# Kernel optimization log

Measured on AMD Instinct MI355X. Metric: run time of the kernel, lower is better.

Reference implementation:

```python
import jax, jax.numpy as jnp
import numpy as np

HEADS = 4
EPS = 1e-5

def _layernorm(x, g, b):
    mu = jnp.mean(x, axis=-1, keepdims=True)
    var = jnp.var(x, axis=-1, keepdims=True)
    return (x - mu) / jnp.sqrt(var + EPS) * g + b

def setup_inputs() -> dict:
    key = jax.random.key(0)
    ks = jax.random.split(key, 16)
    N, dim, k, G = 400000, 256, 1, 4096
    h = jax.random.normal(ks[0], (N, dim), dtype=jnp.float32)
    batch = jnp.sort(jax.random.randint(ks[1], (N,), 0, G).astype(jnp.int64))
    s = 1.0 / np.sqrt(dim)
    return {
        "h": h,
        "batch": batch,
        "num_graphs": G,
        "seed": jax.random.normal(ks[2], (k, dim), dtype=jnp.float32),
        "in_proj_w": jax.random.uniform(ks[3], (3 * dim, dim), minval=-s, maxval=s, dtype=jnp.float32),
        "in_proj_b": jnp.zeros((3 * dim,), jnp.float32),
        "out_w": jax.random.uniform(ks[4], (dim, dim), minval=-s, maxval=s, dtype=jnp.float32),
        "out_b": jnp.zeros((dim,), jnp.float32),
        "w1": jax.random.uniform(ks[5], (4 * dim, dim), minval=-s, maxval=s, dtype=jnp.float32),
        "b1": jnp.zeros((4 * dim,), jnp.float32),
        "w2": jax.random.uniform(ks[6], (dim, 4 * dim), minval=-1.0 / np.sqrt(4 * dim), maxval=1.0 / np.sqrt(4 * dim), dtype=jnp.float32),
        "b2": jnp.zeros((dim,), jnp.float32),
        "g1": jnp.ones((dim,), jnp.float32),
        "beta1": jnp.zeros((dim,), jnp.float32),
        "g2": jnp.ones((dim,), jnp.float32),
        "beta2": jnp.zeros((dim,), jnp.float32),
    }

def reference(h, batch, num_graphs, seed, in_proj_w, in_proj_b, out_w, out_b,
              w1, b1, w2, b2, g1, beta1, g2, beta2):
    N, dim = h.shape
    k = seed.shape[0]
    hd = dim // HEADS
    G = num_graphs
    # q/k/v projections (torch MHA packed in_proj: rows [0:dim]=Q, [dim:2dim]=K, [2dim:]=V)
    q = seed @ in_proj_w[:dim].T + in_proj_b[:dim]                 # [k, dim]
    kk = h @ in_proj_w[dim:2 * dim].T + in_proj_b[dim:2 * dim]     # [N, dim]
    vv = h @ in_proj_w[2 * dim:].T + in_proj_b[2 * dim:]           # [N, dim]
    qh = q.reshape(k, HEADS, hd).transpose(1, 0, 2)                # [H, k, hd]
    kh = kk.reshape(N, HEADS, hd)                                  # [N, H, hd]
    vh = vv.reshape(N, HEADS, hd)                                  # [N, H, hd]
    scale = 1.0 / np.sqrt(hd)
    scores = jnp.einsum('hkd,nhd->nhk', qh, kh) * scale            # [N, H, k]
    # segment softmax over nodes of each graph
    smax = jax.ops.segment_max(scores, batch, num_segments=G)      # [G, H, k]
    e = jnp.exp(scores - smax[batch])                              # [N, H, k]
    denom = jax.ops.segment_sum(e, batch, num_segments=G)          # [G, H, k]
    wv = jax.ops.segment_sum(e[:, :, :, None] * vh[:, :, None, :], batch, num_segments=G)  # [G, H, k, hd]
    attn = jnp.where(denom[..., None] > 0, wv / jnp.maximum(denom, 1e-9)[..., None], 0.0)
    attn = attn.transpose(0, 2, 1, 3).reshape(G, k, dim)           # [G, k, dim]
    o = attn @ out_w.T + out_b                                     # [G, k, dim]
    x = _layernorm(o + seed[None, :, :], g1, beta1)
    f = jax.nn.relu(x @ w1.T + b1) @ w2.T + b2
    x = _layernorm(x + f, g2, beta2)
    # empty graphs output zeros (matches torch loop)
    count = jax.ops.segment_sum(jnp.ones((N,), jnp.float32), batch, num_segments=G)
    return jnp.where((count > 0)[:, None, None], x, 0.0)
```

## Files before the change

### kernel.cpp

```cpp
#include <hip/hip_runtime.h>
#include <hip/hip_bf16.h>


#define DIM 256
#define CHUNK 16

typedef short bf16x8 __attribute__((ext_vector_type(8)));
typedef float f32x4  __attribute__((ext_vector_type(4)));
#define MFMA16(a, b, c) __builtin_amdgcn_mfma_f32_16x16x32_bf16(a, b, c, 0, 0, 0)

#define GLOAD_LDS16(gp, lp)                                          \
    __builtin_amdgcn_global_load_lds(                                \
        (const __attribute__((address_space(1))) void*)(gp),         \
        (__attribute__((address_space(3))) void*)(lp), 16, 0, 0)

#define OFF_C      0
#define OFF_D      1024
#define OFF_CONST  1040
#define OFF_P2B    2048
#define OFF_W1B    133120
#define OFF_W2B    264192
#define OFF_TB     395264
#define OFF_CNT    6162432
#define OFF_STARTS 6166528

__global__ __launch_bounds__(256) void prep_all_kernel(
    const float* __restrict__ seed, const float* __restrict__ ipw,
    const float* __restrict__ ipb, const float* __restrict__ out_w,
    const float* __restrict__ out_b, const float* __restrict__ w1,
    const float* __restrict__ w2, const int* __restrict__ batch,
    float* __restrict__ cvec, float* __restrict__ dconst,
    float* __restrict__ constvec, __hip_bfloat16* __restrict__ P2b,
    __hip_bfloat16* __restrict__ w1b, __hip_bfloat16* __restrict__ w2b,
    int* __restrict__ starts, int N, int G)
{
    int b = blockIdx.x, t = threadIdx.x;
    __shared__ float q_s[DIM];
    if (b < 1024) {
        int i = b >> 2, hD = b & 3;
        float a = 0.f;
        for (int j = 0; j < 64; ++j)
            a += out_w[i * DIM + hD * 64 + j]
               * ipw[(size_t)(2 * DIM + hD * 64 + j) * DIM + t];
        P2b[(size_t)i * 1024 + hD * DIM + t] = __float2bfloat16(a);
    } else if (b == 1024) {
        const float scale = 0.125f;
        float acc = ipb[t];
        for (int d = 0; d < DIM; ++d) acc += seed[d] * ipw[t * DIM + d];
        q_s[t] = acc;
        __syncthreads();
        for (int hh = 0; hh < 4; ++hh) {
            float a = 0.f;
            for (int j = 0; j < 64; ++j)
                a += q_s[hh * 64 + j] * ipw[(size_t)(DIM + hh * 64 + j) * DIM + t];
            cvec[hh * DIM + t] = a * scale;
        }
        if (t < 4) {
            float a = 0.f;
            for (int j = 0; j < 64; ++j)
                a += q_s[t * 64 + j] * ipb[DIM + t * 64 + j];
            dconst[t] = a * scale;
        }
        float cc = out_b[t];
        for (int c = 0; c < DIM; ++c)
            cc += out_w[t * DIM + c] * ipb[2 * DIM + c];
        constvec[t] = cc;
    } else if (b < 1153) {
        int base = (b - 1025) * 2048 + t;
        for (int i = 0; i < 8; ++i)
            w1b[base + i * 256] = __float2bfloat16(w1[base + i * 256]);
    } else if (b < 1281) {
        int base = (b - 1153) * 2048 + t;
        for (int i = 0; i < 8; ++i)
            w2b[base + i * 256] = __float2bfloat16(w2[base + i * 256]);
    } else {
        int n = (b - 1281) * 256 + t;
        if (n < N) {
            int bn = batch[n];
            int bp = (n == 0) ? -1 : batch[n - 1];
            for (int gg = bp + 1; gg <= bn; ++gg) starts[gg] = n;
            if (n == N - 1)
                for (int gg = bn + 1; gg <= G; ++gg) starts[gg] = N;
        }
    }
}

__global__ __launch_bounds__(256) void attn_pool_kernel(
    const float* __restrict__ hmat, const int* __restrict__ starts,
    const float* __restrict__ cvec, const float* __restrict__ dconst,
    __hip_bfloat16* __restrict__ Tb, int* __restrict__ cnt)
{
    int g = blockIdx.x;
    int tid = threadIdx.x;
    int lane = tid & 63, wave = tid >> 6;

    __shared__ float hbuf[4][2][4][DIM];
    __shared__ float lred[4][4];

    int s = starts[g], e = starts[g + 1];
    if (tid == 0) cnt[g] = e - s;
    size_t tbase = (size_t)g * 1024;
    if (e == s) {
        __hip_bfloat16 z = __float2bfloat16(0.f);
        Tb[tbase + tid] = z; Tb[tbase + 256 + tid] = z;
        Tb[tbase + 512 + tid] = z; Tb[tbase + 768 + tid] = z;
        return;
    }

    int hh = lane & 3, seg = lane >> 2;
    const float* cb = cvec + hh * DIM + seg * 16;
    float4 cr0 = *(const float4*)(cb + 0);
    float4 cr1 = *(const float4*)(cb + 4);
    float4 cr2 = *(const float4*)(cb + 8);
    float4 cr3 = *(const float4*)(cb + 12);
    float dc_mine = dconst[hh];

    float S00 = 0.f, S01 = 0.f, S02 = 0.f, S03 = 0.f;
    float S10 = 0.f, S11 = 0.f, S12 = 0.f, S13 = 0.f;
    float S20 = 0.f, S21 = 0.f, S22 = 0.f, S23 = 0.f;
    float S30 = 0.f, S31 = 0.f, S32 = 0.f, S33 = 0.f;
    float lp = 0.f;

    int rows0 = wave * 4;

#pragma unroll
    for (int i = 0; i < 4; ++i) {
        int r = min(s + rows0 + i, e - 1);
        GLOAD_LDS16(&hmat[(size_t)r * DIM + lane * 4], &hbuf[wave][0][i][0]);
    }

    int cur = 0;
    for (int n0 = s; n0 < e; n0 += CHUNK, cur ^= 1) {
        int ccnt = min(CHUNK, e - n0);
        int n1 = n0 + CHUNK;
#pragma unroll
        for (int i = 0; i < 4; ++i) {
            int r = min(n1 + rows0 + i, e - 1);
            GLOAD_LDS16(&hmat[(size_t)r * DIM + lane * 4],
                        &hbuf[wave][cur ^ 1][i][0]);
        }
        asm volatile("s_waitcnt vmcnt(4)" ::: "memory");
        __builtin_amdgcn_sched_barrier(0);

        int nmine = min(max(ccnt - rows0, 0), 4);
        for (int j = 0; j < nmine; ++j) {
            const float* hb = &hbuf[wave][cur][j][0];
            const float* hs = hb + seg * 16;
            float4 h0 = *(const float4*)(hs + 0);
            float4 h1 = *(const float4*)(hs + 4);
            float4 h2 = *(const float4*)(hs + 8);
            float4 h3 = *(const float4*)(hs + 12);
            float p = h0.x * cr0.x + h0.y * cr0.y + h0.z * cr0.z + h0.w * cr0.w
                    + h1.x * cr1.x + h1.y * cr1.y + h1.z * cr1.z + h1.w * cr1.w
                    + h2.x * cr2.x + h2.y * cr2.y + h2.z * cr2.z + h2.w * cr2.w
                    + h3.x * cr3.x + h3.y * cr3.y + h3.z * cr3.z + h3.w * cr3.w;
            p += __shfl_xor(p, 4);
            p += __shfl_xor(p, 8);
            p += __shfl_xor(p, 16);
            p += __shfl_xor(p, 32);
            float ev = __expf(p + dc_mine);
            lp += ev;
            float e0 = __shfl(ev, 0), e1 = __shfl(ev, 1);
            float e2 = __shfl(ev, 2), e3 = __shfl(ev, 3);
            float v0 = hb[lane], v1 = hb[64 + lane];
            float v2 = hb[128 + lane], v3 = hb[192 + lane];
            S00 = fmaf(e0, v0, S00); S01 = fmaf(e0, v1, S01);
            S02 = fmaf(e0, v2, S02); S03 = fmaf(e0, v3, S03);
            S10 = fmaf(e1, v0, S10); S11 = fmaf(e1, v1, S11);
            S12 = fmaf(e1, v2, S12); S13 = fmaf(e1, v3, S13);
            S20 = fmaf(e2, v0, S20); S21 = fmaf(e2, v1, S21);
            S22 = fmaf(e2, v2, S22); S23 = fmaf(e2, v3, S23);
            S30 = fmaf(e3, v0, S30); S31 = fmaf(e3, v1, S31);
            S32 = fmaf(e3, v2, S32); S33 = fmaf(e3, v3, S33);
        }
    }

    asm volatile("s_waitcnt vmcnt(0)" ::: "memory");
    __builtin_amdgcn_sched_barrier(0);
    __syncthreads();
    float* part = &hbuf[0][0][0][0];
#define PIDX(w_, h_, c_) ((((w_) * 4 + (h_)) * 4 + (c_)) * 64 + lane)
    part[PIDX(wave, 0, 0)] = S00; part[PIDX(wave, 0, 1)] = S01;
    part[PIDX(wave, 0, 2)] = S02; part[PIDX(wave, 0, 3)] = S03;
    part[PIDX(wave, 1, 0)] = S10; part[PIDX(wave, 1, 1)] = S11;
    part[PIDX(wave, 1, 2)] = S12; part[PIDX(wave, 1, 3)] = S13;
    part[PIDX(wave, 2, 0)] = S20; part[PIDX(wave, 2, 1)] = S21;
    part[PIDX(wave, 2, 2)] = S22; part[PIDX(wave, 2, 3)] = S23;
    part[PIDX(wave, 3, 0)] = S30; part[PIDX(wave, 3, 1)] = S31;
    part[PIDX(wave, 3, 2)] = S32; part[PIDX(wave, 3, 3)] = S33;
#undef PIDX
    if (lane < 4) lred[wave][lane] = lp;
    __syncthreads();

    int cg = tid >> 6, ln = tid & 63;
#pragma unroll
    for (int h = 0; h < 4; ++h) {
        int base = (h * 4 + cg) * 64 + ln;
        float sum = part[base] + part[base + 1024]
                  + part[base + 2048] + part[base + 3072];
        float den = lred[0][h] + lred[1][h] + lred[2][h] + lred[3][h];
        Tb[tbase + h * 256 + tid] = __float2bfloat16(sum / den);
    }
}

__global__ __launch_bounds__(1024) void mlp_fused_kernel(
    const __hip_bfloat16* __restrict__ Tb, const __hip_bfloat16* __restrict__ P2b,
    const float* __restrict__ constvec, const float* __restrict__ seed,
    const float* __restrict__ g1, const float* __restrict__ be1,
    const __hip_bfloat16* __restrict__ w1b, const float* __restrict__ b1,
    const __hip_bfloat16* __restrict__ w2b, const float* __restrict__ b2,
    const float* __restrict__ g2, const float* __restrict__ be2,
    const int* __restrict__ cnt, float* __restrict__ outp)
{
    int m0 = blockIdx.x * 16;
    int tid = threadIdx.x;
    int w = tid >> 6, lane = tid & 63, quad = lane >> 4, l16 = lane & 15;

    __shared__ float x1s[16][260];
    __shared__ __hip_bfloat16 x1bs[16][264];
    __shared__ __hip_bfloat16 us[16][1032];
    __shared__ float redS[16][16], redQ[16][16];

    f32x4 acc0 = (f32x4){0.f, 0.f, 0.f, 0.f};
    const __hip_bfloat16* Ap0 = Tb + (size_t)(m0 + l16) * 1024 + quad * 8;
    const __hip_bfloat16* Bp0 = P2b + (size_t)(w * 16 + l16) * 1024 + quad * 8;
#pragma unroll 4
    for (int k0 = 0; k0 < 1024; k0 += 32) {
        bf16x8 a = *(const bf16x8*)(Ap0 + k0);
        bf16x8 b = *(const bf16x8*)(Bp0 + k0);
        acc0 = MFMA16(a, b, acc0);
    }
    float v0[4];
    {
        int col = w * 16 + l16;
        float cv = constvec[col] + seed[col];
        float sum[4], sq[4];
#pragma unroll
        for (int r = 0; r < 4; ++r) {
            float x = acc0[r] + cv;
            v0[r] = x; sum[r] = x; sq[r] = x * x;
        }
#pragma unroll
        for (int r = 0; r < 4; ++r) {
            float s_ = sum[r], q_ = sq[r];
            s_ += __shfl_xor(s_, 1);  q_ += __shfl_xor(q_, 1);
            s_ += __shfl_xor(s_, 2);  q_ += __shfl_xor(q_, 2);
            s_ += __shfl_xor(s_, 4);  q_ += __shfl_xor(q_, 4);
            s_ += __shfl_xor(s_, 8);  q_ += __shfl_xor(q_, 8);
            if (l16 == 0) { redS[w][quad * 4 + r] = s_; redQ[w][quad * 4 + r] = q_; }
        }
    }
    __syncthreads();
    {
        float mu_r[4], rs_r[4];
#pragma unroll
        for (int r = 0; r < 4; ++r) {
            int row = quad * 4 + r;
            float s_ = 0.f, q_ = 0.f;
#pragma unroll
            for (int ww = 0; ww < 16; ++ww) { s_ += redS[ww][row]; q_ += redQ[ww][row]; }
            float mu = s_ * (1.f / 256);
            float var = q_ * (1.f / 256) - mu * mu;
            mu_r[r] = mu;
            rs_r[r] = rsqrtf(fmaxf(var, 0.f) + 1e-5f);
        }
        int col = w * 16 + l16;
        float gg = g1[col], bb = be1[col];
#pragma unroll
        for (int r = 0; r < 4; ++r) {
            int row = quad * 4 + r;
            float y = (v0[r] - mu_r[r]) * rs_r[r] * gg + bb;
            x1s[row][col] = y;
            x1bs[row][col] = __float2bfloat16(y);
        }
    }
    __syncthreads();

    f32x4 acc1[4];
#pragma unroll
    for (int i = 0; i < 4; ++i) acc1[i] = (f32x4){0.f, 0.f, 0.f, 0.f};
    const __hip_bfloat16* Bp1 = w1b + (size_t)(w * 64 + l16) * 256 + quad * 8;
#pragma unroll
    for (int k0 = 0; k0 < 256; k0 += 32) {
        bf16x8 a = *(const bf16x8*)&x1bs[l16][quad * 8 + k0];
#pragma unroll
        for (int nt = 0; nt < 4; ++nt) {
            bf16x8 b = *(const bf16x8*)(Bp1 + (size_t)nt * 16 * 256 + k0);
            acc1[nt] = MFMA16(a, b, acc1[nt]);
        }
    }
#pragma unroll
    for (int nt = 0; nt < 4; ++nt) {
        int col = w * 64 + nt * 16 + l16;
        float bb = b1[col];
#pragma unroll
        for (int r = 0; r < 4; ++r) {
            int row = quad * 4 + r;
            us[row][col] = __float2bfloat16(fmaxf(acc1[nt][r] + bb, 0.f));
        }
    }
    __syncthreads();

    f32x4 acc2 = (f32x4){0.f, 0.f, 0.f, 0.f};
    const __hip_bfloat16* Bp2 = w2b + (size_t)(w * 16 + l16) * 1024 + quad * 8;
#pragma unroll 4
    for (int k0 = 0; k0 < 1024; k0 += 32) {
        bf16x8 a = *(const bf16x8*)&us[l16][quad * 8 + k0];
        bf16x8 b = *(const bf16x8*)(Bp2 + k0);
        acc2 = MFMA16(a, b, acc2);
    }
    float v2[4];
    {
        int col = w * 16 + l16;
        float bb = b2[col];
        float sum[4], sq[4];
#pragma unroll
        for (int r = 0; r < 4; ++r) {
            int row = quad * 4 + r;
            float x = acc2[r] + bb + x1s[row][col];
            v2[r] = x; sum[r] = x; sq[r] = x * x;
        }
#pragma unroll
        for (int r = 0; r < 4; ++r) {
            float s_ = sum[r], q_ = sq[r];
            s_ += __shfl_xor(s_, 1);  q_ += __shfl_xor(q_, 1);
            s_ += __shfl_xor(s_, 2);  q_ += __shfl_xor(q_, 2);
            s_ += __shfl_xor(s_, 4);  q_ += __shfl_xor(q_, 4);
            s_ += __shfl_xor(s_, 8);  q_ += __shfl_xor(q_, 8);
            if (l16 == 0) { redS[w][quad * 4 + r] = s_; redQ[w][quad * 4 + r] = q_; }
        }
    }
    __syncthreads();
    {
        int col = w * 16 + l16;
        float gg = g2[col], bb = be2[col];
#pragma unroll
        for (int r = 0; r < 4; ++r) {
            int row = quad * 4 + r;
            float s_ = 0.f, q_ = 0.f;
#pragma unroll
            for (int ww = 0; ww < 16; ++ww) { s_ += redS[ww][row]; q_ += redQ[ww][row]; }
            float mu = s_ * (1.f / 256);
            float var = q_ * (1.f / 256) - mu * mu;
            float rs = rsqrtf(fmaxf(var, 0.f) + 1e-5f);
            int gr = m0 + row;
            float mask = (cnt[gr] > 0) ? 1.f : 0.f;
            float y = ((v2[r] - mu) * rs * gg + bb) * mask;
            outp[(size_t)gr * 256 + col] = y;
        }
    }
}

extern "C" void kernel_launch(void* const* d_in, const int* in_sizes, int n_in,
                              void* d_out, int out_size, void* d_ws, size_t ws_size,
                              hipStream_t stream) {
    const float* h     = (const float*)d_in[0];
    const int*   batch = (const int*)d_in[1];
    const float* seed  = (const float*)d_in[3];
    const float* ipw   = (const float*)d_in[4];
    const float* ipb   = (const float*)d_in[5];
    const float* out_w = (const float*)d_in[6];
    const float* out_b = (const float*)d_in[7];
    const float* w1    = (const float*)d_in[8];
    const float* b1    = (const float*)d_in[9];
    const float* w2    = (const float*)d_in[10];
    const float* b2    = (const float*)d_in[11];
    const float* g1    = (const float*)d_in[12];
    const float* be1   = (const float*)d_in[13];
    const float* g2    = (const float*)d_in[14];
    const float* be2   = (const float*)d_in[15];

    int N = in_sizes[1];
    int G = out_size / DIM;

    float* ws = (float*)d_ws;
    float* cvec     = ws + OFF_C;
    float* dconst   = ws + OFF_D;
    float* constvec = ws + OFF_CONST;
    __hip_bfloat16* P2b = (__hip_bfloat16*)(ws + OFF_P2B);
    __hip_bfloat16* w1b = (__hip_bfloat16*)(ws + OFF_W1B);
    __hip_bfloat16* w2b = (__hip_bfloat16*)(ws + OFF_W2B);
    __hip_bfloat16* Tb  = (__hip_bfloat16*)(ws + OFF_TB);
    int*   cnt      = (int*)(ws + OFF_CNT);
    int*   startsp  = (int*)(ws + OFF_STARTS);

    int sblocks = (N + 255) / 256;
    prep_all_kernel<<<1281 + sblocks, 256, 0, stream>>>(
        seed, ipw, ipb, out_w, out_b, w1, w2, batch,
        cvec, dconst, constvec, P2b, w1b, w2b, startsp, N, G);
    attn_pool_kernel<<<G, 256, 0, stream>>>(h, startsp, cvec, dconst, Tb, cnt);
    mlp_fused_kernel<<<G / 16, 1024, 0, stream>>>(Tb, P2b, constvec, seed, g1, be1,
                                                  w1b, b1, w2b, b2, g2, be2, cnt,
                                                  (float*)d_out);
}
```

Before: 666.0 us.

## Replace per-graph attention pooling with row-parallel scatter using atomics

The per-graph pooling kernel (one block per graph, LDS double-buffered loads, starts computed from batch) is replaced by a row-parallel kernel. Each wave streams 64 consecutive rows, computes all four head scores per row and accumulates exp-weighted sums in registers. It flushes them with atomicAdd to global per-graph accumulators whenever the graph id changes. A small finalize kernel divides by the denominators and writes the bf16 T matrix, and the prep kernel now zeroes the accumulators instead of building segment starts. The aim is to remove load imbalance across uneven graph sizes and the per-graph block overhead. In exchange it adds atomic traffic, leaves only one row load in flight per wave, and makes the summation order non-deterministic.

```diff
diff --git a/kernel.cpp b/kernel.cpp
--- a/kernel.cpp
+++ b/kernel.cpp
@@ -3,16 +3,10 @@
 
 
 #define DIM 256
-#define CHUNK 16
 
 typedef short bf16x8 __attribute__((ext_vector_type(8)));
 typedef float f32x4  __attribute__((ext_vector_type(4)));
 #define MFMA16(a, b, c) __builtin_amdgcn_mfma_f32_16x16x32_bf16(a, b, c, 0, 0, 0)
-
-#define GLOAD_LDS16(gp, lp)                                          \
-    __builtin_amdgcn_global_load_lds(                                \
-        (const __attribute__((address_space(1))) void*)(gp),         \
-        (__attribute__((address_space(3))) void*)(lp), 16, 0, 0)
 
 #define OFF_C      0
 #define OFF_D      1024
@@ -22,17 +16,18 @@
 #define OFF_W2B    264192
 #define OFF_TB     395264
 #define OFF_CNT    6162432
-#define OFF_STARTS 6166528
+#define OFF_SACC   6171648
+#define OFF_DEN    10365952
 
 __global__ __launch_bounds__(256) void prep_all_kernel(
     const float* __restrict__ seed, const float* __restrict__ ipw,
     const float* __restrict__ ipb, const float* __restrict__ out_w,
     const float* __restrict__ out_b, const float* __restrict__ w1,
-    const float* __restrict__ w2, const int* __restrict__ batch,
+    const float* __restrict__ w2,
     float* __restrict__ cvec, float* __restrict__ dconst,
     float* __restrict__ constvec, __hip_bfloat16* __restrict__ P2b,
     __hip_bfloat16* __restrict__ w1b, __hip_bfloat16* __restrict__ w2b,
-    int* __restrict__ starts, int N, int G)
+    float* __restrict__ zbase)
 {
     int b = blockIdx.x, t = threadIdx.x;
     __shared__ float q_s[DIM];
@@ -74,133 +69,110 @@
         for (int i = 0; i < 8; ++i)
             w2b[base + i * 256] = __float2bfloat16(w2[base + i * 256]);
     } else {
-        int n = (b - 1281) * 256 + t;
-        if (n < N) {
-            int bn = batch[n];
-            int bp = (n == 0) ? -1 : batch[n - 1];
-            for (int gg = bp + 1; gg <= bn; ++gg) starts[gg] = n;
-            if (n == N - 1)
-                for (int gg = bn + 1; gg <= G; ++gg) starts[gg] = N;
-        }
-    }
-}
-
-__global__ __launch_bounds__(256) void attn_pool_kernel(
-    const float* __restrict__ hmat, const int* __restrict__ starts,
+        int zb = b - 1281;
+        float4* z = (float4*)zbase + (size_t)zb * 1024;
+        float4 zero = {0.f, 0.f, 0.f, 0.f};
+        z[t] = zero; z[t + 256] = zero; z[t + 512] = zero; z[t + 768] = zero;
+    }
+}
+
+__global__ __launch_bounds__(256) void attn_scatter_kernel(
+    const float* __restrict__ hmat, const int* __restrict__ batch,
     const float* __restrict__ cvec, const float* __restrict__ dconst,
+    float* __restrict__ Sacc, float* __restrict__ denomAcc, int N)
+{
+    int wglob = blockIdx.x * 4 + (threadIdx.x >> 6);
+    int lane = threadIdx.x & 63;
+    int r0 = wglob * 64;
+    if (r0 >= N) return;
+    int rend = min(r0 + 64, N);
+
+    float4 c0 = *(const float4*)&cvec[0 * DIM + 4 * lane];
+    float4 c1 = *(const float4*)&cvec[1 * DIM + 4 * lane];
+    float4 c2 = *(const float4*)&cvec[2 * DIM + 4 * lane];
+    float4 c3 = *(const float4*)&cvec[3 * DIM + 4 * lane];
+    float d0 = dconst[0], d1 = dconst[1], d2 = dconst[2], d3 = dconst[3];
+
+    float4 S0 = {0,0,0,0}, S1 = {0,0,0,0}, S2 = {0,0,0,0}, S3 = {0,0,0,0};
+    float4 lp = {0,0,0,0};
+
+    int gcur = batch[r0];
+    float4 h4 = *(const float4*)&hmat[(size_t)r0 * DIM + 4 * lane];
+
+    for (int r = r0; r < rend; ++r) {
+        float4 hv = h4;
+        int gn = -1;
+        if (r + 1 < rend) {
+            gn = batch[r + 1];
+            h4 = *(const float4*)&hmat[(size_t)(r + 1) * DIM + 4 * lane];
+        }
+        float p0 = hv.x*c0.x + hv.y*c0.y + hv.z*c0.z + hv.w*c0.w;
+        float p1 = hv.x*c1.x + hv.y*c1.y + hv.z*c1.z + hv.w*c1.w;
+        float p2 = hv.x*c2.x + hv.y*c2.y + hv.z*c2.z + hv.w*c2.w;
+        float p3 = hv.x*c3.x + hv.y*c3.y + hv.z*c3.z + hv.w*c3.w;
+        float sA = __shfl_xor((lane & 1) ? p0 : p2, 1);
+        float sB = __shfl_xor((lane & 1) ? p1 : p3, 1);
+        float a  = (lane & 1) ? (p2 + sA) : (p0 + sA);
+        float bb = (lane & 1) ? (p3 + sB) : (p1 + sB);
+        float sC = __shfl_xor((lane & 2) ? a : bb, 2);
+        float v  = (lane & 2) ? (bb + sC) : (a + sC);
+        v += __shfl_xor(v, 4);
+        v += __shfl_xor(v, 8);
+        v += __shfl_xor(v, 16);
+        v += __shfl_xor(v, 32);
+        int q0 = lane & ~3;
+        float sc0 = __shfl(v, q0 + 0);
+        float sc2 = __shfl(v, q0 + 1);
+        float sc1 = __shfl(v, q0 + 2);
+        float sc3 = __shfl(v, q0 + 3);
+        float e0 = __expf(sc0 + d0), e1 = __expf(sc1 + d1);
+        float e2 = __expf(sc2 + d2), e3 = __expf(sc3 + d3);
+        lp.x += e0; lp.y += e1; lp.z += e2; lp.w += e3;
+        S0.x = fmaf(e0, hv.x, S0.x); S0.y = fmaf(e0, hv.y, S0.y);
+        S0.z = fmaf(e0, hv.z, S0.z); S0.w = fmaf(e0, hv.w, S0.w);
+        S1.x = fmaf(e1, hv.x, S1.x); S1.y = fmaf(e1, hv.y, S1.y);
+        S1.z = fmaf(e1, hv.z, S1.z); S1.w = fmaf(e1, hv.w, S1.w);
+        S2.x = fmaf(e2, hv.x, S2.x); S2.y = fmaf(e2, hv.y, S2.y);
+        S2.z = fmaf(e2, hv.z, S2.z); S2.w = fmaf(e2, hv.w, S2.w);
+        S3.x = fmaf(e3, hv.x, S3.x); S3.y = fmaf(e3, hv.y, S3.y);
+        S3.z = fmaf(e3, hv.z, S3.z); S3.w = fmaf(e3, hv.w, S3.w);
+
+        if (gn != gcur) {
+            float* base = Sacc + (size_t)gcur * 1024 + 4 * lane;
+            atomicAdd(base + 0,       S0.x); atomicAdd(base + 1,       S0.y);
+            atomicAdd(base + 2,       S0.z); atomicAdd(base + 3,       S0.w);
+            atomicAdd(base + 256 + 0, S1.x); atomicAdd(base + 256 + 1, S1.y);
+            atomicAdd(base + 256 + 2, S1.z); atomicAdd(base + 256 + 3, S1.w);
+            atomicAdd(base + 512 + 0, S2.x); atomicAdd(base + 512 + 1, S2.y);
+            atomicAdd(base + 512 + 2, S2.z); atomicAdd(base + 512 + 3, S2.w);
+            atomicAdd(base + 768 + 0, S3.x); atomicAdd(base + 768 + 1, S3.y);
+            atomicAdd(base + 768 + 2, S3.z); atomicAdd(base + 768 + 3, S3.w);
+            if (lane < 4) {
+                float lv = (lane == 0) ? lp.x : (lane == 1) ? lp.y
+                         : (lane == 2) ? lp.z : lp.w;
+                atomicAdd(denomAcc + gcur * 4 + lane, lv);
+            }
+            S0 = (float4){0,0,0,0}; S1 = (float4){0,0,0,0};
+            S2 = (float4){0,0,0,0}; S3 = (float4){0,0,0,0};
+            lp = (float4){0,0,0,0};
+            gcur = gn;
+        }
+    }
+}
+
+__global__ __launch_bounds__(256) void finalize_T_kernel(
+    const float* __restrict__ Sacc, const float* __restrict__ denomAcc,
     __hip_bfloat16* __restrict__ Tb, int* __restrict__ cnt)
 {
-    int g = blockIdx.x;
-    int tid = threadIdx.x;
-    int lane = tid & 63, wave = tid >> 6;
-
-    __shared__ float hbuf[4][2][4][DIM];
-    __shared__ float lred[4][4];
-
-    int s = starts[g], e = starts[g + 1];
-    if (tid == 0) cnt[g] = e - s;
-    size_t tbase = (size_t)g * 1024;
-    if (e == s) {
-        __hip_bfloat16 z = __float2bfloat16(0.f);
-        Tb[tbase + tid] = z; Tb[tbase + 256 + tid] = z;
-        Tb[tbase + 512 + tid] = z; Tb[tbase + 768 + tid] = z;
-        return;
-    }
-
-    int hh = lane & 3, seg = lane >> 2;
-    const float* cb = cvec + hh * DIM + seg * 16;
-    float4 cr0 = *(const float4*)(cb + 0);
-    float4 cr1 = *(const float4*)(cb + 4);
-    float4 cr2 = *(const float4*)(cb + 8);
-    float4 cr3 = *(const float4*)(cb + 12);
-    float dc_mine = dconst[hh];
-
-    float S00 = 0.f, S01 = 0.f, S02 = 0.f, S03 = 0.f;
-    float S10 = 0.f, S11 = 0.f, S12 = 0.f, S13 = 0.f;
-    float S20 = 0.f, S21 = 0.f, S22 = 0.f, S23 = 0.f;
-    float S30 = 0.f, S31 = 0.f, S32 = 0.f, S33 = 0.f;
-    float lp = 0.f;
-
-    int rows0 = wave * 4;
-
-#pragma unroll
-    for (int i = 0; i < 4; ++i) {
-        int r = min(s + rows0 + i, e - 1);
-        GLOAD_LDS16(&hmat[(size_t)r * DIM + lane * 4], &hbuf[wave][0][i][0]);
-    }
-
-    int cur = 0;
-    for (int n0 = s; n0 < e; n0 += CHUNK, cur ^= 1) {
-        int ccnt = min(CHUNK, e - n0);
-        int n1 = n0 + CHUNK;
-#pragma unroll
-        for (int i = 0; i < 4; ++i) {
-            int r = min(n1 + rows0 + i, e - 1);
-            GLOAD_LDS16(&hmat[(size_t)r * DIM + lane * 4],
-                        &hbuf[wave][cur ^ 1][i][0]);
-        }
-        asm volatile("s_waitcnt vmcnt(4)" ::: "memory");
-        __builtin_amdgcn_sched_barrier(0);
-
-        int nmine = min(max(ccnt - rows0, 0), 4);
-        for (int j = 0; j < nmine; ++j) {
-            const float* hb = &hbuf[wave][cur][j][0];
-            const float* hs = hb + seg * 16;
-            float4 h0 = *(const float4*)(hs + 0);
-            float4 h1 = *(const float4*)(hs + 4);
-            float4 h2 = *(const float4*)(hs + 8);
-            float4 h3 = *(const float4*)(hs + 12);
-            float p = h0.x * cr0.x + h0.y * cr0.y + h0.z * cr0.z + h0.w * cr0.w
-                    + h1.x * cr1.x + h1.y * cr1.y + h1.z * cr1.z + h1.w * cr1.w
-                    + h2.x * cr2.x + h2.y * cr2.y + h2.z * cr2.z + h2.w * cr2.w
-                    + h3.x * cr3.x + h3.y * cr3.y + h3.z * cr3.z + h3.w * cr3.w;
-            p += __shfl_xor(p, 4);
-            p += __shfl_xor(p, 8);
-            p += __shfl_xor(p, 16);
-            p += __shfl_xor(p, 32);
-            float ev = __expf(p + dc_mine);
-            lp += ev;
-            float e0 = __shfl(ev, 0), e1 = __shfl(ev, 1);
-            float e2 = __shfl(ev, 2), e3 = __shfl(ev, 3);
-            float v0 = hb[lane], v1 = hb[64 + lane];
-            float v2 = hb[128 + lane], v3 = hb[192 + lane];
-            S00 = fmaf(e0, v0, S00); S01 = fmaf(e0, v1, S01);
-            S02 = fmaf(e0, v2, S02); S03 = fmaf(e0, v3, S03);
-            S10 = fmaf(e1, v0, S10); S11 = fmaf(e1, v1, S11);
-            S12 = fmaf(e1, v2, S12); S13 = fmaf(e1, v3, S13);
-            S20 = fmaf(e2, v0, S20); S21 = fmaf(e2, v1, S21);
-            S22 = fmaf(e2, v2, S22); S23 = fmaf(e2, v3, S23);
-            S30 = fmaf(e3, v0, S30); S31 = fmaf(e3, v1, S31);
-            S32 = fmaf(e3, v2, S32); S33 = fmaf(e3, v3, S33);
-        }
-    }
-
-    asm volatile("s_waitcnt vmcnt(0)" ::: "memory");
-    __builtin_amdgcn_sched_barrier(0);
-    __syncthreads();
-    float* part = &hbuf[0][0][0][0];
-#define PIDX(w_, h_, c_) ((((w_) * 4 + (h_)) * 4 + (c_)) * 64 + lane)
-    part[PIDX(wave, 0, 0)] = S00; part[PIDX(wave, 0, 1)] = S01;
-    part[PIDX(wave, 0, 2)] = S02; part[PIDX(wave, 0, 3)] = S03;
-    part[PIDX(wave, 1, 0)] = S10; part[PIDX(wave, 1, 1)] = S11;
-    part[PIDX(wave, 1, 2)] = S12; part[PIDX(wave, 1, 3)] = S13;
-    part[PIDX(wave, 2, 0)] = S20; part[PIDX(wave, 2, 1)] = S21;
-    part[PIDX(wave, 2, 2)] = S22; part[PIDX(wave, 2, 3)] = S23;
-    part[PIDX(wave, 3, 0)] = S30; part[PIDX(wave, 3, 1)] = S31;
-    part[PIDX(wave, 3, 2)] = S32; part[PIDX(wave, 3, 3)] = S33;
-#undef PIDX
-    if (lane < 4) lred[wave][lane] = lp;
-    __syncthreads();
-
-    int cg = tid >> 6, ln = tid & 63;
-#pragma unroll
-    for (int h = 0; h < 4; ++h) {
-        int base = (h * 4 + cg) * 64 + ln;
-        float sum = part[base] + part[base + 1024]
-                  + part[base + 2048] + part[base + 3072];
-        float den = lred[0][h] + lred[1][h] + lred[2][h] + lred[3][h];
-        Tb[tbase + h * 256 + tid] = __float2bfloat16(sum / den);
-    }
+    int g = blockIdx.x, t = threadIdx.x;
+    float4 den = *(const float4*)&denomAcc[g * 4];
+    if (t == 0) cnt[g] = (den.x > 0.f) ? 1 : 0;
+    const float* sb = Sacc + (size_t)g * 1024;
+    size_t tb = (size_t)g * 1024;
+    Tb[tb + t]       = __float2bfloat16(den.x > 0.f ? sb[t]       / den.x : 0.f);
+    Tb[tb + 256 + t] = __float2bfloat16(den.y > 0.f ? sb[256 + t] / den.y : 0.f);
+    Tb[tb + 512 + t] = __float2bfloat16(den.z > 0.f ? sb[512 + t] / den.z : 0.f);
+    Tb[tb + 768 + t] = __float2bfloat16(den.w > 0.f ? sb[768 + t] / den.w : 0.f);
 }
 
 __global__ __launch_bounds__(1024) void mlp_fused_kernel(
@@ -382,13 +354,16 @@
     __hip_bfloat16* w2b = (__hip_bfloat16*)(ws + OFF_W2B);
     __hip_bfloat16* Tb  = (__hip_bfloat16*)(ws + OFF_TB);
     int*   cnt      = (int*)(ws + OFF_CNT);
-    int*   startsp  = (int*)(ws + OFF_STARTS);
-
-    int sblocks = (N + 255) / 256;
-    prep_all_kernel<<<1281 + sblocks, 256, 0, stream>>>(
-        seed, ipw, ipb, out_w, out_b, w1, w2, batch,
-        cvec, dconst, constvec, P2b, w1b, w2b, startsp, N, G);
-    attn_pool_kernel<<<G, 256, 0, stream>>>(h, startsp, cvec, dconst, Tb, cnt);
+    float* Sacc     = ws + OFF_SACC;
+    float* denomAcc = ws + OFF_DEN;
+
+    prep_all_kernel<<<2309, 256, 0, stream>>>(
+        seed, ipw, ipb, out_w, out_b, w1, w2,
+        cvec, dconst, constvec, P2b, w1b, w2b, Sacc );
+    int ablocks = (N + 255) / 256;
+    attn_scatter_kernel<<<ablocks, 256, 0, stream>>>(h, batch, cvec, dconst,
+                                                     Sacc, denomAcc, N);
+    finalize_T_kernel<<<G, 256, 0, stream>>>(Sacc, denomAcc, Tb, cnt);
     mlp_fused_kernel<<<G / 16, 1024, 0, stream>>>(Tb, P2b, constvec, seed, g1, be1,
                                                   w1b, b1, w2b, b2, g2, be2, cnt,
                                                   (float*)d_out);
```

New measurement: 736.3 us. +10.6%, slower.
